# Kernel tuning notes

Hardware: AMD Instinct MI355X
Metric: run time of the kernel (lower is better)

The kernel has to match this reference:

```python
import jax, jax.numpy as jnp
import numpy as np
import itertools

# Hyperparameters (match HashGrid4D defaults)
BASE, MAXRES, NLEV, F = 512, 32768, 8, 4
SCALE = 2.0 ** (np.log2(MAXRES / BASE) / (NLEV - 1))
RES = [int(np.floor(BASE * SCALE ** l)) for l in range(NLEV)]  # 512 .. 32768
TRES = 25
LOG2_STATIC = 19
LOG2_DYN = (14, 12, 12)
PRIMES = np.array([1, 2654435761, 805459861], dtype=np.uint32)


def _offsets(D):
    # binary corner offsets of the D-dim hypercube: [2^D, D]
    return jnp.asarray(np.array(list(itertools.product((0, 1), repeat=D)), dtype=np.uint32))


def hash_encode(x, table, log2_size):
    """Multi-resolution hash-grid encoding.
    x: [N, D] in [0,1); table: [NLEV, 2^log2_size, F] -> [N, NLEV*F]."""
    N, D = x.shape
    offs = _offsets(D)                                   # [2^D, D]
    mask = np.uint32((1 << log2_size) - 1)
    feats = []
    for l in range(NLEV):
        pos = x * RES[l]                                 # [N, D]
        p0f = jnp.floor(pos)
        frac = pos - p0f                                 # [N, D]
        p0 = p0f.astype(jnp.uint32)
        corners = p0[:, None, :] + offs[None]            # [N, 2^D, D]
        h = corners[..., 0] * PRIMES[0]
        for d in range(1, D):
            h = h ^ (corners[..., d] * PRIMES[d])        # spatial hash (tcnn primes)
        idx = (h & mask).astype(jnp.int32)               # [N, 2^D]
        # trilinear/bilinear weights
        w = jnp.prod(jnp.where(offs[None] == 1, frac[:, None, :], 1.0 - frac[:, None, :]), axis=-1)
        feats.append(jnp.sum(table[l][idx] * w[..., None], axis=1))  # [N, F]
    return jnp.concatenate(feats, axis=-1)               # [N, NLEV*F]


def hash_t(x, tables, t, log2_size):
    """Time-interpolated 2D hash encoding (HashGridT).
    tables: [TRES, NLEV, 2^log2_size, F]; t: scalar in [0,1]."""
    idx = t * (TRES - 1)
    i1 = jnp.floor(idx).astype(jnp.int32)
    i2 = jnp.ceil(idx).astype(jnp.int32)
    frac = idx - i1                                      # 0 when i1 == i2
    f1 = hash_encode(x, tables[i1], log2_size)
    f2 = hash_encode(x, tables[i2], log2_size)
    return (1.0 - frac) * f1 + frac * f2


def setup_inputs() -> dict:
    key = jax.random.key(0)
    ks = jax.random.split(key, 6)
    N = 1_000_000
    x = jax.random.uniform(ks[0], (N, 3), dtype=jnp.float32)
    t = jax.random.uniform(ks[1], (1,), dtype=jnp.float32)
    init = lambda k, shape: jax.random.uniform(k, shape, dtype=jnp.float32, minval=-1e-4, maxval=1e-4)
    static_table = init(ks[2], (NLEV, 1 << LOG2_STATIC, F))
    table_xy = init(ks[3], (TRES, NLEV, 1 << LOG2_DYN[0], F))
    table_xz = init(ks[4], (TRES, NLEV, 1 << LOG2_DYN[1], F))
    table_yz = init(ks[5], (TRES, NLEV, 1 << LOG2_DYN[2], F))
    return {"x": x, "t": t, "static_table": static_table,
            "table_xy": table_xy, "table_xz": table_xz, "table_yz": table_yz}


def reference(x, t, static_table, table_xy, table_xz, table_yz):
    ts = t[0]
    feat_static = hash_encode(x, static_table, LOG2_STATIC)        # [N, 32]
    xy = x[:, [0, 1]]
    xz = x[:, [0, 2]]
    yz = x[:, [1, 2]]
    feat_dynamic = (hash_t(xy, table_xy, ts, LOG2_DYN[0])
                    * hash_t(xz, table_xz, ts, LOG2_DYN[1])
                    * hash_t(yz, table_yz, ts, LOG2_DYN[2]))       # [N, 32]
    return feat_static, feat_dynamic
```

## Files before the change

kernel.cpp:

```cpp
#include <hip/hip_runtime.h>
#include <math.h>
#include <stdint.h>

#define NLEV 8

#define SBF_ENT (8u << 19)
#define XY_ENT (8u << 14)
#define XZ_ENT (8u << 12)
#define YZ_ENT (8u << 12)
#define WS_ENT (XY_ENT + XZ_ENT + YZ_ENT)
#define WS_BYTES_BF16 ((size_t)SBF_ENT * 8 + (size_t)WS_ENT * 8)

typedef float nf4 __attribute__((ext_vector_type(4)));

__device__ __forceinline__ void nt_store4(float4 v, float4* dst) {
    nf4 t = { v.x, v.y, v.z, v.w };
    __builtin_nontemporal_store(t, (nf4*)dst);
}

__device__ __forceinline__ unsigned short bf16rne(float f) {
    uint32_t u = __float_as_uint(f);
    uint32_t r = u + 0x7FFFu + ((u >> 16) & 1u);
    return (unsigned short)(r >> 16);
}

__device__ __forceinline__ float bf2f(unsigned short s) {
    return __uint_as_float((uint32_t)s << 16);
}

struct ResParams { int res[NLEV]; };

__global__ __launch_bounds__(256) void convert_bf16_kernel(
    const float4* __restrict__ stat, ushort4* __restrict__ sbf)
{
    uint32_t i = blockIdx.x * blockDim.x + threadIdx.x;
    if (i >= SBF_ENT) return;
    float4 v = stat[i];
    ushort4 o;
    o.x = bf16rne(v.x); o.y = bf16rne(v.y);
    o.z = bf16rne(v.z); o.w = bf16rne(v.w);
    sbf[i] = o;
}

__global__ __launch_bounds__(256) void prelerp_bf16_kernel(
    const float* __restrict__ tarr,
    const float4* __restrict__ txy,
    const float4* __restrict__ txz,
    const float4* __restrict__ tyz,
    ushort4* __restrict__ ws)
{
    uint32_t e = blockIdx.x * blockDim.x + threadIdx.x;
    if (e >= WS_ENT) return;

    float ts  = tarr[0];
    float ti  = ts * 24.0f;
    float i1f = floorf(ti);
    float tf  = ti - i1f;
    int i1 = (int)i1f;
    int i2 = (int)ceilf(ti);
    float w1 = 1.0f - tf;

    const float4* src1;
    const float4* src2;
    uint32_t off;
    if (e < XY_ENT) {
        off = e;
        src1 = txy + (size_t)i1 * XY_ENT + off;
        src2 = txy + (size_t)i2 * XY_ENT + off;
    } else if (e < XY_ENT + XZ_ENT) {
        off = e - XY_ENT;
        src1 = txz + (size_t)i1 * XZ_ENT + off;
        src2 = txz + (size_t)i2 * XZ_ENT + off;
    } else {
        off = e - (XY_ENT + XZ_ENT);
        src1 = tyz + (size_t)i1 * YZ_ENT + off;
        src2 = tyz + (size_t)i2 * YZ_ENT + off;
    }
    float4 v1 = *src1, v2 = *src2;
    ushort4 o;
    o.x = bf16rne(w1 * v1.x + tf * v2.x);
    o.y = bf16rne(w1 * v1.y + tf * v2.y);
    o.z = bf16rne(w1 * v1.z + tf * v2.z);
    o.w = bf16rne(w1 * v1.w + tf * v2.w);
    ws[e] = o;
}

__global__ __launch_bounds__(256) void static_level_kernel(
    const float* __restrict__ x,
    const ushort4* __restrict__ st,
    float4* __restrict__ out,
    int N, int l, float res)
{
    int p = blockIdx.x * 256 + threadIdx.x;
    if (p >= N) return;

    float x0 = x[p * 3 + 0];
    float x1 = x[p * 3 + 1];
    float x2 = x[p * 3 + 2];

    float pa = x0 * res, pb = x1 * res, pc = x2 * res;
    float fa = floorf(pa), fb = floorf(pb), fc = floorf(pc);
    float ra = pa - fa, rb = pb - fb, rc = pc - fc;
    uint32_t ia = (uint32_t)fa, ib = (uint32_t)fb, ic = (uint32_t)fc;

    uint32_t idx[8];
    float    w[8];
#pragma unroll
    for (int c = 0; c < 8; ++c) {
        uint32_t o0 = (c >> 2) & 1u, o1 = (c >> 1) & 1u, o2 = c & 1u;
        uint32_t h = (ia + o0) ^ ((ib + o1) * 2654435761u) ^ ((ic + o2) * 805459861u);
        idx[c] = h & ((1u << 19) - 1u);
        w[c] = (o0 ? ra : 1.0f - ra) * (o1 ? rb : 1.0f - rb) * (o2 ? rc : 1.0f - rc);
    }

    ushort4 g[8];
#pragma unroll
    for (int c = 0; c < 8; ++c) g[c] = st[idx[c]];

    float4 acc = make_float4(0.f, 0.f, 0.f, 0.f);
#pragma unroll
    for (int c = 0; c < 8; ++c) {
        float wc = w[c];
        acc.x += wc * bf2f(g[c].x);
        acc.y += wc * bf2f(g[c].y);
        acc.z += wc * bf2f(g[c].z);
        acc.w += wc * bf2f(g[c].w);
    }
    nt_store4(acc, &out[(size_t)p * 8 + l]);
}

__device__ __forceinline__ void dyn_point(
    int p, int l, float res,
    const float* __restrict__ x,
    const ushort4* __restrict__ wxy,
    const ushort4* sxz, const ushort4* syz,
    float4* __restrict__ out)
{
    float x0 = x[p * 3 + 0];
    float x1 = x[p * 3 + 1];
    float x2 = x[p * 3 + 2];

    uint32_t ixy[4], ixz[4], iyz[4];
    float    wxy_[4], wxz_[4], wyz_[4];

    {
        float pa = x0 * res, pb = x1 * res;
        float fa = floorf(pa), fb = floorf(pb);
        float ra = pa - fa, rb = pb - fb;
        uint32_t ia = (uint32_t)fa, ib = (uint32_t)fb;
#pragma unroll
        for (int c = 0; c < 4; ++c) {
            uint32_t oa = (c >> 1) & 1u, ob = c & 1u;
            uint32_t h = (ia + oa) ^ ((ib + ob) * 2654435761u);
            ixy[c] = h & ((1u << 14) - 1u);
            wxy_[c] = (oa ? ra : 1.0f - ra) * (ob ? rb : 1.0f - rb);
        }
    }
    {
        float pa = x0 * res, pb = x2 * res;
        float fa = floorf(pa), fb = floorf(pb);
        float ra = pa - fa, rb = pb - fb;
        uint32_t ia = (uint32_t)fa, ib = (uint32_t)fb;
#pragma unroll
        for (int c = 0; c < 4; ++c) {
            uint32_t oa = (c >> 1) & 1u, ob = c & 1u;
            uint32_t h = (ia + oa) ^ ((ib + ob) * 2654435761u);
            ixz[c] = h & ((1u << 12) - 1u);
            wxz_[c] = (oa ? ra : 1.0f - ra) * (ob ? rb : 1.0f - rb);
        }
    }
    {
        float pa = x1 * res, pb = x2 * res;
        float fa = floorf(pa), fb = floorf(pb);
        float ra = pa - fa, rb = pb - fb;
        uint32_t ia = (uint32_t)fa, ib = (uint32_t)fb;
#pragma unroll
        for (int c = 0; c < 4; ++c) {
            uint32_t oa = (c >> 1) & 1u, ob = c & 1u;
            uint32_t h = (ia + oa) ^ ((ib + ob) * 2654435761u);
            iyz[c] = h & ((1u << 12) - 1u);
            wyz_[c] = (oa ? ra : 1.0f - ra) * (ob ? rb : 1.0f - rb);
        }
    }

    ushort4 exy[4];
#pragma unroll
    for (int c = 0; c < 4; ++c) exy[c] = wxy[ixy[c]];
    ushort4 exz[4], eyz[4];
#pragma unroll
    for (int c = 0; c < 4; ++c) exz[c] = sxz[ixz[c]];
#pragma unroll
    for (int c = 0; c < 4; ++c) eyz[c] = syz[iyz[c]];

    float4 f0 = make_float4(0.f, 0.f, 0.f, 0.f);
    float4 f1 = make_float4(0.f, 0.f, 0.f, 0.f);
    float4 f2 = make_float4(0.f, 0.f, 0.f, 0.f);
#pragma unroll
    for (int c = 0; c < 4; ++c) {
        float wc = wxy_[c];
        f0.x += wc * bf2f(exy[c].x); f0.y += wc * bf2f(exy[c].y);
        f0.z += wc * bf2f(exy[c].z); f0.w += wc * bf2f(exy[c].w);
    }
#pragma unroll
    for (int c = 0; c < 4; ++c) {
        float wc = wxz_[c];
        f1.x += wc * bf2f(exz[c].x); f1.y += wc * bf2f(exz[c].y);
        f1.z += wc * bf2f(exz[c].z); f1.w += wc * bf2f(exz[c].w);
    }
#pragma unroll
    for (int c = 0; c < 4; ++c) {
        float wc = wyz_[c];
        f2.x += wc * bf2f(eyz[c].x); f2.y += wc * bf2f(eyz[c].y);
        f2.z += wc * bf2f(eyz[c].z); f2.w += wc * bf2f(eyz[c].w);
    }

    float4 d;
    d.x = f0.x * f1.x * f2.x;
    d.y = f0.y * f1.y * f2.y;
    d.z = f0.z * f1.z * f2.z;
    d.w = f0.w * f1.w * f2.w;
    nt_store4(d, &out[(size_t)p * 8 + l]);
}

__global__ __launch_bounds__(256) void dynamic_lds_kernel(
    const float* __restrict__ x,
    const ushort4* __restrict__ ws,
    float4* __restrict__ out,
    int N, ResParams rp)
{
    __shared__ ushort4 sxz[4096];
    __shared__ ushort4 syz[4096];
    int l      = blockIdx.x & 7;
    int chunk  = blockIdx.x >> 3;
    int nchunk = gridDim.x >> 3;

    const ushort4* wxz = ws + XY_ENT + ((size_t)l << 12);
    const ushort4* wyz = ws + XY_ENT + XZ_ENT + ((size_t)l << 12);
    for (int i = threadIdx.x; i < 4096; i += 256) {
        sxz[i] = wxz[i];
        syz[i] = wyz[i];
    }
    __syncthreads();

    const ushort4* wxy = ws + ((size_t)l << 14);
    float res = (float)rp.res[l];
    int stride = nchunk * 256;
    int start  = chunk * 256 + threadIdx.x;

    for (int p = start; p < N; p += 2 * stride) {
        int p2 = p + stride;
        dyn_point(p, l, res, x, wxy, sxz, syz, out);
        if (p2 < N) dyn_point(p2, l, res, x, wxy, sxz, syz, out);
    }
}

__device__ __forceinline__ float4 plane_feat2(const float4* __restrict__ t1,
                                              const float4* __restrict__ t2,
                                              float a, float b, float tf,
                                              float res, uint32_t mask)
{
    float pa = a * res, pb = b * res;
    float fa = floorf(pa), fb = floorf(pb);
    float ra = pa - fa, rb = pb - fb;
    uint32_t ia = (uint32_t)fa, ib = (uint32_t)fb;
    float w1s = 1.0f - tf;
    float4 acc = make_float4(0.f, 0.f, 0.f, 0.f);
#pragma unroll
    for (int c = 0; c < 4; ++c) {
        uint32_t oa = (c >> 1) & 1u, ob = c & 1u;
        uint32_t h = (ia + oa) ^ ((ib + ob) * 2654435761u);
        uint32_t idx = h & mask;
        float4 v1 = t1[idx];
        float4 v2 = t2[idx];
        float w = (oa ? ra : 1.0f - ra) * (ob ? rb : 1.0f - rb);
        float wa = w * w1s, wb = w * tf;
        acc.x += wa * v1.x + wb * v2.x;
        acc.y += wa * v1.y + wb * v2.y;
        acc.z += wa * v1.z + wb * v2.z;
        acc.w += wa * v1.w + wb * v2.w;
    }
    return acc;
}

__global__ __launch_bounds__(256) void fused_fallback_kernel(
    const float* __restrict__ x,
    const float* __restrict__ tarr,
    const float4* __restrict__ stat,
    const float4* __restrict__ txy,
    const float4* __restrict__ txz,
    const float4* __restrict__ tyz,
    float4* __restrict__ out,
    int N, ResParams rp)
{
    int tid = blockIdx.x * blockDim.x + threadIdx.x;
    if (tid >= N * NLEV) return;
    int p = tid >> 3;
    int l = tid & 7;

    float x0 = x[p * 3 + 0];
    float x1 = x[p * 3 + 1];
    float x2 = x[p * 3 + 2];

    float ts  = tarr[0];
    float ti  = ts * 24.0f;
    float i1f = floorf(ti);
    float i2f = ceilf(ti);
    float tf  = ti - i1f;
    int i1 = (int)i1f, i2 = (int)i2f;

    float res = (float)rp.res[l];

    float p0 = x0 * res, p1 = x1 * res, p2 = x2 * res;
    float f0 = floorf(p0), f1 = floorf(p1), f2 = floorf(p2);
    float r0 = p0 - f0, r1 = p1 - f1, r2 = p2 - f2;
    uint32_t i0 = (uint32_t)f0, j0 = (uint32_t)f1, k0 = (uint32_t)f2;
    const float4* st = stat + ((size_t)l << 19);
    float4 acc = make_float4(0.f, 0.f, 0.f, 0.f);
#pragma unroll
    for (int c = 0; c < 8; ++c) {
        uint32_t o0 = (c >> 2) & 1u, o1 = (c >> 1) & 1u, o2 = c & 1u;
        uint32_t h = (i0 + o0) ^ ((j0 + o1) * 2654435761u) ^ ((k0 + o2) * 805459861u);
        uint32_t idx = h & ((1u << 19) - 1u);
        float4 v = st[idx];
        float w = (o0 ? r0 : 1.0f - r0) * (o1 ? r1 : 1.0f - r1) * (o2 ? r2 : 1.0f - r2);
        acc.x += w * v.x; acc.y += w * v.y; acc.z += w * v.z; acc.w += w * v.w;
    }
    out[(size_t)p * 8 + l] = acc;

    const float4* xy1 = txy + (((size_t)i1 * 8 + l) << 14);
    const float4* xy2 = txy + (((size_t)i2 * 8 + l) << 14);
    const float4* xz1 = txz + (((size_t)i1 * 8 + l) << 12);
    const float4* xz2 = txz + (((size_t)i2 * 8 + l) << 12);
    const float4* yz1 = tyz + (((size_t)i1 * 8 + l) << 12);
    const float4* yz2 = tyz + (((size_t)i2 * 8 + l) << 12);

    float4 fxy = plane_feat2(xy1, xy2, x0, x1, tf, res, (1u << 14) - 1u);
    float4 fxz = plane_feat2(xz1, xz2, x0, x2, tf, res, (1u << 12) - 1u);
    float4 fyz = plane_feat2(yz1, yz2, x1, x2, tf, res, (1u << 12) - 1u);

    float4 d;
    d.x = fxy.x * fxz.x * fyz.x;
    d.y = fxy.y * fxz.y * fyz.y;
    d.z = fxy.z * fxz.z * fyz.z;
    d.w = fxy.w * fxz.w * fyz.w;
    out[(size_t)N * 8 + (size_t)p * 8 + l] = d;
}

extern "C" void kernel_launch(void* const* d_in, const int* in_sizes, int n_in,
                              void* d_out, int out_size, void* d_ws, size_t ws_size,
                              hipStream_t stream)
{
    const float*  x    = (const float*)d_in[0];
    const float*  t    = (const float*)d_in[1];
    const float4* stat = (const float4*)d_in[2];
    const float4* txy  = (const float4*)d_in[3];
    const float4* txz  = (const float4*)d_in[4];
    const float4* tyz  = (const float4*)d_in[5];

    int N = in_sizes[0] / 3;

    ResParams rp;
    double scale = pow(2.0, 6.0 / 7.0);
    for (int l = 0; l < NLEV; ++l)
        rp.res[l] = (int)floor(512.0 * pow(scale, (double)l));

    if (ws_size >= WS_BYTES_BF16) {
        ushort4* sbf     = (ushort4*)d_ws;
        ushort4* dynlerp = (ushort4*)((char*)d_ws + (size_t)SBF_ENT * 8);

        hipLaunchKernelGGL(convert_bf16_kernel,
                           dim3((SBF_ENT + 255) / 256), dim3(256), 0, stream,
                           stat, sbf);
        hipLaunchKernelGGL(prelerp_bf16_kernel,
                           dim3((WS_ENT + 255) / 256), dim3(256), 0, stream,
                           t, txy, txz, tyz, dynlerp);

        int sgrid = (N + 255) / 256;
        for (int l = 0; l < NLEV; ++l) {
            hipLaunchKernelGGL(static_level_kernel,
                               dim3(sgrid), dim3(256), 0, stream,
                               x, sbf + ((size_t)l << 19), (float4*)d_out,
                               N, l, (float)rp.res[l]);
        }

        hipLaunchKernelGGL(dynamic_lds_kernel,
                           dim3(512), dim3(256), 0, stream,
                           x, (const ushort4*)dynlerp,
                           (float4*)d_out + (size_t)N * 8, N, rp);
    } else {
        hipLaunchKernelGGL(fused_fallback_kernel,
                           dim3((N * NLEV + 255) / 256), dim3(256), 0, stream,
                           x, t, stat, txy, txz, tyz, (float4*)d_out, N, rp);
    }
}
```

Before: 676.3 us.

## Split dynamic kernel so xy table lives in LDS; nontemporal static gathers

The dynamic encoding is split into two kernels. The first stages the full 128 KB xy table for one level in LDS and writes the xy feature to the output. The second keeps xz/yz in LDS, reads the partial result back and multiplies in the other two planes. The static gather also switches to 64-bit nontemporal loads with inline bf16 unpacking. This trades global gathers from the xy table for an extra output write and read-back plus an extra launch, and the 128 KB LDS block limits occupancy to about one block per CU.

```diff
diff --git a/kernel.cpp b/kernel.cpp
--- a/kernel.cpp
+++ b/kernel.cpp
@@ -113,116 +113,78 @@
         w[c] = (o0 ? ra : 1.0f - ra) * (o1 ? rb : 1.0f - rb) * (o2 ? rc : 1.0f - rc);
     }
 
-    ushort4 g[8];
-#pragma unroll
-    for (int c = 0; c < 8; ++c) g[c] = st[idx[c]];
+    unsigned long long g[8];
+#pragma unroll
+    for (int c = 0; c < 8; ++c)
+        g[c] = __builtin_nontemporal_load(
+                   (const unsigned long long*)(st + idx[c]));
 
     float4 acc = make_float4(0.f, 0.f, 0.f, 0.f);
 #pragma unroll
     for (int c = 0; c < 8; ++c) {
         float wc = w[c];
-        acc.x += wc * bf2f(g[c].x);
-        acc.y += wc * bf2f(g[c].y);
-        acc.z += wc * bf2f(g[c].z);
-        acc.w += wc * bf2f(g[c].w);
+        uint32_t lo = (uint32_t)g[c];
+        uint32_t hi = (uint32_t)(g[c] >> 32);
+        acc.x += wc * __uint_as_float(lo << 16);
+        acc.y += wc * __uint_as_float(lo & 0xffff0000u);
+        acc.z += wc * __uint_as_float(hi << 16);
+        acc.w += wc * __uint_as_float(hi & 0xffff0000u);
     }
     nt_store4(acc, &out[(size_t)p * 8 + l]);
 }
 
-__device__ __forceinline__ void dyn_point(
-    int p, int l, float res,
+__global__ __launch_bounds__(256) void dyn_xy_kernel(
     const float* __restrict__ x,
-    const ushort4* __restrict__ wxy,
-    const ushort4* sxz, const ushort4* syz,
-    float4* __restrict__ out)
-{
-    float x0 = x[p * 3 + 0];
-    float x1 = x[p * 3 + 1];
-    float x2 = x[p * 3 + 2];
-
-    uint32_t ixy[4], ixz[4], iyz[4];
-    float    wxy_[4], wxz_[4], wyz_[4];
-
-    {
+    const ushort4* __restrict__ ws,
+    float4* __restrict__ out,
+    int N, ResParams rp)
+{
+    __shared__ ushort4 sxy[16384];
+    int l      = blockIdx.x & 7;
+    int chunk  = blockIdx.x >> 3;
+    int nchunk = gridDim.x >> 3;
+
+    const ushort4* wxy = ws + ((size_t)l << 14);
+    for (int i = threadIdx.x; i < 16384; i += 256) sxy[i] = wxy[i];
+    __syncthreads();
+
+    float res = (float)rp.res[l];
+    int stride = nchunk * 256;
+
+    for (int p = chunk * 256 + threadIdx.x; p < N; p += stride) {
+        float x0 = x[p * 3 + 0];
+        float x1 = x[p * 3 + 1];
+
         float pa = x0 * res, pb = x1 * res;
         float fa = floorf(pa), fb = floorf(pb);
         float ra = pa - fa, rb = pb - fb;
         uint32_t ia = (uint32_t)fa, ib = (uint32_t)fb;
+
+        uint32_t id[4];
+        float    w[4];
 #pragma unroll
         for (int c = 0; c < 4; ++c) {
             uint32_t oa = (c >> 1) & 1u, ob = c & 1u;
             uint32_t h = (ia + oa) ^ ((ib + ob) * 2654435761u);
-            ixy[c] = h & ((1u << 14) - 1u);
-            wxy_[c] = (oa ? ra : 1.0f - ra) * (ob ? rb : 1.0f - rb);
-        }
-    }
-    {
-        float pa = x0 * res, pb = x2 * res;
-        float fa = floorf(pa), fb = floorf(pb);
-        float ra = pa - fa, rb = pb - fb;
-        uint32_t ia = (uint32_t)fa, ib = (uint32_t)fb;
+            id[c] = h & ((1u << 14) - 1u);
+            w[c] = (oa ? ra : 1.0f - ra) * (ob ? rb : 1.0f - rb);
+        }
+        ushort4 e[4];
+#pragma unroll
+        for (int c = 0; c < 4; ++c) e[c] = sxy[id[c]];
+
+        float4 f = make_float4(0.f, 0.f, 0.f, 0.f);
 #pragma unroll
         for (int c = 0; c < 4; ++c) {
-            uint32_t oa = (c >> 1) & 1u, ob = c & 1u;
-            uint32_t h = (ia + oa) ^ ((ib + ob) * 2654435761u);
-            ixz[c] = h & ((1u << 12) - 1u);
-            wxz_[c] = (oa ? ra : 1.0f - ra) * (ob ? rb : 1.0f - rb);
-        }
-    }
-    {
-        float pa = x1 * res, pb = x2 * res;
-        float fa = floorf(pa), fb = floorf(pb);
-        float ra = pa - fa, rb = pb - fb;
-        uint32_t ia = (uint32_t)fa, ib = (uint32_t)fb;
-#pragma unroll
-        for (int c = 0; c < 4; ++c) {
-            uint32_t oa = (c >> 1) & 1u, ob = c & 1u;
-            uint32_t h = (ia + oa) ^ ((ib + ob) * 2654435761u);
-            iyz[c] = h & ((1u << 12) - 1u);
-            wyz_[c] = (oa ? ra : 1.0f - ra) * (ob ? rb : 1.0f - rb);
-        }
-    }
-
-    ushort4 exy[4];
-#pragma unroll
-    for (int c = 0; c < 4; ++c) exy[c] = wxy[ixy[c]];
-    ushort4 exz[4], eyz[4];
-#pragma unroll
-    for (int c = 0; c < 4; ++c) exz[c] = sxz[ixz[c]];
-#pragma unroll
-    for (int c = 0; c < 4; ++c) eyz[c] = syz[iyz[c]];
-
-    float4 f0 = make_float4(0.f, 0.f, 0.f, 0.f);
-    float4 f1 = make_float4(0.f, 0.f, 0.f, 0.f);
-    float4 f2 = make_float4(0.f, 0.f, 0.f, 0.f);
-#pragma unroll
-    for (int c = 0; c < 4; ++c) {
-        float wc = wxy_[c];
-        f0.x += wc * bf2f(exy[c].x); f0.y += wc * bf2f(exy[c].y);
-        f0.z += wc * bf2f(exy[c].z); f0.w += wc * bf2f(exy[c].w);
-    }
-#pragma unroll
-    for (int c = 0; c < 4; ++c) {
-        float wc = wxz_[c];
-        f1.x += wc * bf2f(exz[c].x); f1.y += wc * bf2f(exz[c].y);
-        f1.z += wc * bf2f(exz[c].z); f1.w += wc * bf2f(exz[c].w);
-    }
-#pragma unroll
-    for (int c = 0; c < 4; ++c) {
-        float wc = wyz_[c];
-        f2.x += wc * bf2f(eyz[c].x); f2.y += wc * bf2f(eyz[c].y);
-        f2.z += wc * bf2f(eyz[c].z); f2.w += wc * bf2f(eyz[c].w);
-    }
-
-    float4 d;
-    d.x = f0.x * f1.x * f2.x;
-    d.y = f0.y * f1.y * f2.y;
-    d.z = f0.z * f1.z * f2.z;
-    d.w = f0.w * f1.w * f2.w;
-    nt_store4(d, &out[(size_t)p * 8 + l]);
-}
-
-__global__ __launch_bounds__(256) void dynamic_lds_kernel(
+            float wc = w[c];
+            f.x += wc * bf2f(e[c].x); f.y += wc * bf2f(e[c].y);
+            f.z += wc * bf2f(e[c].z); f.w += wc * bf2f(e[c].w);
+        }
+        out[(size_t)p * 8 + l] = f;
+    }
+}
+
+__global__ __launch_bounds__(256) void dyn_xzyz_kernel(
     const float* __restrict__ x,
     const ushort4* __restrict__ ws,
     float4* __restrict__ out,
@@ -242,15 +204,72 @@
     }
     __syncthreads();
 
-    const ushort4* wxy = ws + ((size_t)l << 14);
     float res = (float)rp.res[l];
     int stride = nchunk * 256;
-    int start  = chunk * 256 + threadIdx.x;
-
-    for (int p = start; p < N; p += 2 * stride) {
-        int p2 = p + stride;
-        dyn_point(p, l, res, x, wxy, sxz, syz, out);
-        if (p2 < N) dyn_point(p2, l, res, x, wxy, sxz, syz, out);
+
+    for (int p = chunk * 256 + threadIdx.x; p < N; p += stride) {
+        float x0 = x[p * 3 + 0];
+        float x1 = x[p * 3 + 1];
+        float x2 = x[p * 3 + 2];
+
+        uint32_t ixz[4], iyz[4];
+        float    wxz_[4], wyz_[4];
+        {
+            float pa = x0 * res, pb = x2 * res;
+            float fa = floorf(pa), fb = floorf(pb);
+            float ra = pa - fa, rb = pb - fb;
+            uint32_t ia = (uint32_t)fa, ib = (uint32_t)fb;
+#pragma unroll
+            for (int c = 0; c < 4; ++c) {
+                uint32_t oa = (c >> 1) & 1u, ob = c & 1u;
+                uint32_t h = (ia + oa) ^ ((ib + ob) * 2654435761u);
+                ixz[c] = h & ((1u << 12) - 1u);
+                wxz_[c] = (oa ? ra : 1.0f - ra) * (ob ? rb : 1.0f - rb);
+            }
+        }
+        {
+            float pa = x1 * res, pb = x2 * res;
+            float fa = floorf(pa), fb = floorf(pb);
+            float ra = pa - fa, rb = pb - fb;
+            uint32_t ia = (uint32_t)fa, ib = (uint32_t)fb;
+#pragma unroll
+            for (int c = 0; c < 4; ++c) {
+                uint32_t oa = (c >> 1) & 1u, ob = c & 1u;
+                uint32_t h = (ia + oa) ^ ((ib + ob) * 2654435761u);
+                iyz[c] = h & ((1u << 12) - 1u);
+                wyz_[c] = (oa ? ra : 1.0f - ra) * (ob ? rb : 1.0f - rb);
+            }
+        }
+
+        float4 prev = out[(size_t)p * 8 + l];
+
+        ushort4 exz[4], eyz[4];
+#pragma unroll
+        for (int c = 0; c < 4; ++c) exz[c] = sxz[ixz[c]];
+#pragma unroll
+        for (int c = 0; c < 4; ++c) eyz[c] = syz[iyz[c]];
+
+        float4 f1 = make_float4(0.f, 0.f, 0.f, 0.f);
+        float4 f2 = make_float4(0.f, 0.f, 0.f, 0.f);
+#pragma unroll
+        for (int c = 0; c < 4; ++c) {
+            float wc = wxz_[c];
+            f1.x += wc * bf2f(exz[c].x); f1.y += wc * bf2f(exz[c].y);
+            f1.z += wc * bf2f(exz[c].z); f1.w += wc * bf2f(exz[c].w);
+        }
+#pragma unroll
+        for (int c = 0; c < 4; ++c) {
+            float wc = wyz_[c];
+            f2.x += wc * bf2f(eyz[c].x); f2.y += wc * bf2f(eyz[c].y);
+            f2.z += wc * bf2f(eyz[c].z); f2.w += wc * bf2f(eyz[c].w);
+        }
+
+        float4 d;
+        d.x = prev.x * f1.x * f2.x;
+        d.y = prev.y * f1.y * f2.y;
+        d.z = prev.z * f1.z * f2.z;
+        d.w = prev.w * f1.w * f2.w;
+        nt_store4(d, &out[(size_t)p * 8 + l]);
     }
 }
 
@@ -383,10 +402,13 @@
                                N, l, (float)rp.res[l]);
         }
 
-        hipLaunchKernelGGL(dynamic_lds_kernel,
+        float4* dyn_out = (float4*)d_out + (size_t)N * 8;
+        hipLaunchKernelGGL(dyn_xy_kernel,
+                           dim3(256), dim3(256), 0, stream,
+                           x, (const ushort4*)dynlerp, dyn_out, N, rp);
+        hipLaunchKernelGGL(dyn_xzyz_kernel,
                            dim3(512), dim3(256), 0, stream,
-                           x, (const ushort4*)dynlerp,
-                           (float4*)d_out + (size_t)N * 8, N, rp);
+                           x, (const ushort4*)dynlerp, dyn_out, N, rp);
     } else {
         hipLaunchKernelGGL(fused_fallback_kernel,
                            dim3((N * NLEV + 255) / 256), dim3(256), 0, stream,
```

New measurement: 1.460 ms. +115.8%, slower.
